# Kernel tuning notes

Measured on AMD Instinct MI355X. Metric: run time of the kernel, lower is better.

Reference implementation:

```python
import jax, jax.numpy as jnp
import numpy as np

D_MODEL, D_K, D_V, HEAD = 512, 512, 512, 8
SCALE = 1.0 / np.sqrt(D_K)  # torch code divides by sqrt(d_k) (full d_k, not head_dim)
NEG = -1.0e9


def setup_inputs() -> dict:
    key = jax.random.key(0)
    ks = jax.random.split(key, 10)
    B, S = 2, 4096
    x = jax.random.normal(ks[0], (B, S, D_MODEL), dtype=jnp.float32)
    mask = jax.random.randint(ks[1], (B, S), 0, 2, dtype=jnp.int32)
    s = 1.0 / np.sqrt(D_MODEL)
    Wq = jax.random.normal(ks[2], (D_MODEL, D_K), dtype=jnp.float32) * s
    bq = jnp.zeros((D_K,), jnp.float32)
    Wk = jax.random.normal(ks[3], (D_MODEL, D_K), dtype=jnp.float32) * s
    bk = jnp.zeros((D_K,), jnp.float32)
    Wv = jax.random.normal(ks[4], (D_MODEL, D_V), dtype=jnp.float32) * s
    bv = jnp.zeros((D_V,), jnp.float32)
    Wo = jax.random.normal(ks[5], (D_V, D_MODEL), dtype=jnp.float32) * s
    bo = jnp.zeros((D_MODEL,), jnp.float32)
    return {"x": x, "mask": mask, "Wq": Wq, "bq": bq, "Wk": Wk, "bk": bk,
            "Wv": Wv, "bv": bv, "Wo": Wo, "bo": bo}


def reference(x, mask, Wq, bq, Wk, bk, Wv, bv, Wo, bo):
    B, S, _ = x.shape
    hd_k = D_K // HEAD
    hd_v = D_V // HEAD
    # projections -> [B, H, S, hd]
    Q = (x @ Wq + bq).reshape(B, S, HEAD, hd_k).transpose(0, 2, 1, 3)
    K = (x @ Wk + bk).reshape(B, S, HEAD, hd_k).transpose(0, 2, 1, 3)
    V = (x @ Wv + bv).reshape(B, S, HEAD, hd_v).transpose(0, 2, 1, 3)
    # scores [B, H, S, S], scaled by 1/sqrt(d_k) (full d_k, faithful to source)
    scores = jnp.einsum('bhqd,bhkd->bhqk', Q, K) * SCALE
    m = (mask == 1)[:, None, None, :]  # [B,1,1,S]
    scores = jnp.where(m, NEG, scores)
    attn = jax.nn.softmax(scores, axis=-1)
    out = jnp.einsum('bhqk,bhkd->bhqd', attn, V)  # [B,H,S,hd_v]
    out = out.transpose(0, 2, 1, 3).reshape(B, S, D_V)
    return out @ Wo + bo
```

## Files before the change

### kernel.cpp

```cpp
#include <hip/hip_runtime.h>
#include <hip/hip_bf16.h>
#include <stdint.h>

typedef __attribute__((ext_vector_type(8))) short bf16x8;
typedef __attribute__((ext_vector_type(4))) float f32x4;
typedef __attribute__((ext_vector_type(16))) float f32x16;
typedef __attribute__((ext_vector_type(4))) unsigned int u32x4;

#define MFMA16(a, b, c) __builtin_amdgcn_mfma_f32_16x16x32_bf16(a, b, c, 0, 0, 0)
#define MFMA32(a, b, c) __builtin_amdgcn_mfma_f32_32x32x16_bf16(a, b, c, 0, 0, 0)

constexpr float QSCALE = 0.04419417382415922f * 1.4426950408889634f;

__device__ __forceinline__ void gload_lds16(const void* g, void* l) {
  __builtin_amdgcn_global_load_lds((const __attribute__((address_space(1))) uint32_t*)g,
                                   (__attribute__((address_space(3))) uint32_t*)l, 16, 0, 0);
}
__device__ __forceinline__ bf16x8 lds_read_swz(const short* base, int row, int ch) {
  return *(const bf16x8*)((const char*)base + row * 128 + (((ch ^ row) & 7) << 4));
}
__device__ __forceinline__ short f2b(float f) {
  __hip_bfloat16 h = __float2bfloat16(f);
  return *reinterpret_cast<short*>(&h);
}
__device__ __forceinline__ float exp2fast(float x) {
#if __has_builtin(__builtin_amdgcn_exp2f)
  return __builtin_amdgcn_exp2f(x);
#else
  return exp2f(x);
#endif
}

__global__ void k_cvt_x(const float* __restrict__ x, short* __restrict__ xb) {
  const int i = blockIdx.x * 256 + threadIdx.x;
  const float4 v = ((const float4*)x)[i];
  short4 o;
  o.x = f2b(v.x); o.y = f2b(v.y); o.z = f2b(v.z); o.w = f2b(v.w);
  ((short4*)xb)[i] = o;
}

__global__ void k_cvt_w(const float* __restrict__ wq, const float* __restrict__ wk,
                        const float* __restrict__ wv, const float* __restrict__ wo,
                        short* __restrict__ wt) {
  const int gid = blockIdx.x * 256 + threadIdx.x;
  const int mat = gid >> 18;
  const int idx = gid & 262143;
  const int n = idx >> 9, k = idx & 511;
  const float* w = (mat == 0) ? wq : (mat == 1) ? wk : (mat == 2) ? wv : wo;
  wt[gid] = f2b(w[k * 512 + n]);
}

__global__ void k_scan(const int* __restrict__ mask, int* __restrict__ perm,
                       int* __restrict__ cnt) {
  __shared__ int ws[16];
  const int b = blockIdx.x, tid = threadIdx.x;
  const int lane = tid & 63, w = tid >> 6;
  const int* m = mask + b * 4096;
  int v[4], s = 0;
#pragma unroll
  for (int j = 0; j < 4; ++j) { v[j] = (m[tid * 4 + j] == 0) ? 1 : 0; s += v[j]; }
  int sc = s;
  for (int d = 1; d < 64; d <<= 1) { int t = __shfl_up(sc, d); if (lane >= d) sc += t; }
  if (lane == 63) ws[w] = sc;
  __syncthreads();
  if (tid == 0) {
    int acc = 0;
    for (int i = 0; i < 16; ++i) { int t = ws[i]; ws[i] = acc; acc += t; }
    cnt[b] = acc;
  }
  __syncthreads();
  int pos = ws[w] + sc - s;
  int* p = perm + b * 4096;
#pragma unroll
  for (int j = 0; j < 4; ++j) { p[tid * 4 + j] = v[j] ? pos : -1; pos += v[j]; }
}

__global__ __launch_bounds__(256, 2) void k_gemmqkv(
    const short* __restrict__ A, const short* __restrict__ W,
    const float* __restrict__ bq, const float* __restrict__ bk,
    const float* __restrict__ bv, const int* __restrict__ perm,
    short* __restrict__ oq, short* __restrict__ ok, short* __restrict__ ov) {
  __shared__ short Asm[2][128 * 64];
  __shared__ short Bsm[2][128 * 64];
  const int tid = threadIdx.x;
  const int wave = tid >> 6, lane = tid & 63;
  const int lane15 = lane & 15, g = lane >> 4;
  const int wm = wave >> 1, wn = wave & 1;
  const int m0 = blockIdx.x * 128;
  const int n0 = blockIdx.y * 128;

  const char* Ag = (const char*)A + (size_t)m0 * 1024;
  const char* Bg = (const char*)W + (size_t)n0 * 1024;

  f32x4 acc[4][4] = {};

  auto stage = [&](int buf, int kt) {
    const int k0b = kt * 128;
#pragma unroll
    for (int q = 0; q < 4; ++q) {
      int s_ = (wave * 4 + q) * 64 + lane;
      int row = s_ >> 3, ch = s_ & 7;
      gload_lds16(Ag + (size_t)row * 1024 + k0b + (((ch ^ row) & 7) << 4),
                  (char*)&Asm[buf][0] + s_ * 16);
      gload_lds16(Bg + (size_t)row * 1024 + k0b + (((ch ^ row) & 7) << 4),
                  (char*)&Bsm[buf][0] + s_ * 16);
    }
  };

  stage(0, 0);
  asm volatile("s_waitcnt vmcnt(0)" ::: "memory");
  __syncthreads();

  for (int kt = 0; kt < 8; ++kt) {
    const int cur = kt & 1;
    if (kt < 7) stage(cur ^ 1, kt + 1);
#pragma unroll
    for (int kk = 0; kk < 2; ++kk) {
      bf16x8 af[4], bfr[4];
#pragma unroll
      for (int m = 0; m < 4; ++m)
        af[m] = lds_read_swz(&Asm[cur][0], wm * 64 + m * 16 + lane15, kk * 4 + g);
#pragma unroll
      for (int n = 0; n < 4; ++n)
        bfr[n] = lds_read_swz(&Bsm[cur][0], wn * 64 + n * 16 + lane15, kk * 4 + g);
      __builtin_amdgcn_s_setprio(1);
#pragma unroll
      for (int m = 0; m < 4; ++m)
#pragma unroll
        for (int n = 0; n < 4; ++n)
          acc[m][n] = MFMA16(af[m], bfr[n], acc[m][n]);
      __builtin_amdgcn_s_setprio(0);
    }
    asm volatile("s_waitcnt vmcnt(0)" ::: "memory");
    __syncthreads();
  }

#pragma unroll
  for (int nf = 0; nf < 4; ++nf) {
    const int col = n0 + wn * 64 + nf * 16 + lane15;
    const int mat = col >> 9, nn = col & 511;
    const int hh = nn >> 6, d = nn & 63;
    const float bias = ((mat == 0) ? bq : (mat == 1) ? bk : bv)[nn];
    const int dk = d >> 4, hb = (d >> 3) & 1, jj = d & 7;
#pragma unroll
    for (int mf = 0; mf < 4; ++mf) {
#pragma unroll
      for (int j = 0; j < 4; ++j) {
        const int rowg = m0 + wm * 64 + mf * 16 + g * 4 + j;
        const int b_ = rowg >> 12, sl = rowg & 4095;
        const size_t bh = (size_t)(b_ * 8 + hh);
        const float v = acc[mf][nf][j] + bias;
        if (mat == 0) {
          oq[bh * 262144 +
             (size_t)(((sl >> 5) * 4 + dk) * 64 + hb * 32 + (sl & 31)) * 8 + jj] =
              f2b(v * QSCALE);
        } else {
          const int pm_ = perm[b_ * 4096 + sl];
          if (pm_ >= 0) {
            const int t = pm_ >> 6, r = pm_ & 63;
            if (mat == 1) {
              ok[bh * 262144 +
                 (size_t)((t * 8 + dk * 2 + (r >> 5)) * 64 + hb * 32 + (r & 31)) * 8 + jj] =
                  f2b(v);
            } else {
              const int mm = (r & ~12) | (((r >> 2) & 1) << 3) | (((r >> 3) & 1) << 2);
              ov[bh * 262144 +
                 (size_t)((t * 8 + ((mm >> 4) & 3) * 2 + (d >> 5)) * 64 +
                          ((mm >> 3) & 1) * 32 + (d & 31)) * 8 + (mm & 7)] = f2b(v);
            }
          }
        }
      }
    }
  }
}

__global__ __launch_bounds__(256, 2) void k_gemmo(
    const short* __restrict__ A, const short* __restrict__ W,
    const float* __restrict__ bias, float* __restrict__ fo) {
  __shared__ short Asm[2][128 * 64];
  __shared__ short Bsm[2][64 * 64];
  const int tid = threadIdx.x;
  const int wave = tid >> 6, lane = tid & 63;
  const int lane15 = lane & 15, g = lane >> 4;
  const int wm = wave >> 1, wn = wave & 1;
  const int m0 = blockIdx.x * 128;
  const int n0 = blockIdx.y * 64;

  const char* Ag = (const char*)A + (size_t)m0 * 1024;
  const char* Bg = (const char*)W + (size_t)n0 * 1024;

  f32x4 acc[4][2] = {};

  auto stage = [&](int buf, int kt) {
    const int k0b = kt * 128;
#pragma unroll
    for (int q = 0; q < 4; ++q) {
      int s_ = (wave * 4 + q) * 64 + lane;
      int row = s_ >> 3, ch = s_ & 7;
      gload_lds16(Ag + (size_t)row * 1024 + k0b + (((ch ^ row) & 7) << 4),
                  (char*)&Asm[buf][0] + s_ * 16);
    }
#pragma unroll
    for (int q = 0; q < 2; ++q) {
      int s_ = (wave * 2 + q) * 64 + lane;
      int row = s_ >> 3, ch = s_ & 7;
      gload_lds16(Bg + (size_t)row * 1024 + k0b + (((ch ^ row) & 7) << 4),
                  (char*)&Bsm[buf][0] + s_ * 16);
    }
  };

  stage(0, 0);
  asm volatile("s_waitcnt vmcnt(0)" ::: "memory");
  __syncthreads();

  for (int kt = 0; kt < 8; ++kt) {
    const int cur = kt & 1;
    if (kt < 7) stage(cur ^ 1, kt + 1);
#pragma unroll
    for (int kk = 0; kk < 2; ++kk) {
      bf16x8 af[4], bfr[2];
#pragma unroll
      for (int m = 0; m < 4; ++m)
        af[m] = lds_read_swz(&Asm[cur][0], wm * 64 + m * 16 + lane15, kk * 4 + g);
#pragma unroll
      for (int n = 0; n < 2; ++n)
        bfr[n] = lds_read_swz(&Bsm[cur][0], wn * 32 + n * 16 + lane15, kk * 4 + g);
      __builtin_amdgcn_s_setprio(1);
#pragma unroll
      for (int m = 0; m < 4; ++m)
#pragma unroll
        for (int n = 0; n < 2; ++n)
          acc[m][n] = MFMA16(af[m], bfr[n], acc[m][n]);
      __builtin_amdgcn_s_setprio(0);
    }
    asm volatile("s_waitcnt vmcnt(0)" ::: "memory");
    __syncthreads();
  }

#pragma unroll
  for (int nf = 0; nf < 2; ++nf) {
    const int col = n0 + wn * 32 + nf * 16 + lane15;
    const float b = bias[col];
#pragma unroll
    for (int mf = 0; mf < 4; ++mf)
#pragma unroll
      for (int j = 0; j < 4; ++j) {
        const int rowg = m0 + wm * 64 + mf * 16 + g * 4 + j;
        fo[(size_t)rowg * 512 + col] = acc[mf][nf][j] + b;
      }
  }
}

__global__ __launch_bounds__(256, 2) void k_attn(
    const short* __restrict__ Qp, const short* __restrict__ Kp,
    const short* __restrict__ Vp, const int* __restrict__ cnt,
    short* __restrict__ out) {
  __shared__ short Ks[2][8][512];
  __shared__ short Vs[2][8][512];

  const int tid = threadIdx.x;
  const int wave = tid >> 6, lane = tid & 63;
  const int l31 = lane & 31, h = lane >> 5;
  const int bid = blockIdx.x;
  const int sid = (bid & 7) * 64 + (bid >> 3);
  const int qt = sid & 31, bh = sid >> 5;
  const int b = bh >> 3, hh = bh & 7;
  const int qb = qt * 4 + wave;

  const short* Qg = Qp + (size_t)bh * 262144;
  const short* Kg = Kp + (size_t)bh * 262144;
  const short* Vg = Vp + (size_t)bh * 262144;

  bf16x8 qreg[4];
#pragma unroll
  for (int dk = 0; dk < 4; ++dk)
    qreg[dk] = *(const bf16x8*)(Qg + ((size_t)(qb * 4 + dk) * 64 + lane) * 8);

  const int cn = cnt[b];
  const int nt = max(1, (cn + 63) >> 6);
  const int lim = cn - (nt - 1) * 64;

  auto stage = [&](int buf, int t) {
#pragma unroll
    for (int q = 0; q < 2; ++q) {
      const int u = wave * 2 + q;
      gload_lds16(Kg + ((size_t)(t * 8 + u) * 64 + lane) * 8, &Ks[buf][u][lane * 8]);
      gload_lds16(Vg + ((size_t)(t * 8 + u) * 64 + lane) * 8, &Vs[buf][u][lane * 8]);
    }
  };
  auto ldsK = [&](int buf, int u) { return *(const bf16x8*)&Ks[buf][u][lane * 8]; };
  auto ldsV = [&](int buf, int u) { return *(const bf16x8*)&Vs[buf][u][lane * 8]; };

  f32x16 o0 = {}, o1 = {};
  float l_ = 0.f;

  stage(0, 0);
  __syncthreads();

  for (int t = 0; t < nt; ++t) {
    const int cur = t & 1;
    if (t + 1 < nt) stage(cur ^ 1, t + 1);

    f32x16 s0v = {}, s1v = {};
    __builtin_amdgcn_s_setprio(1);
#pragma unroll
    for (int dk = 0; dk < 4; ++dk) {
      s0v = MFMA32(ldsK(cur, 2 * dk), qreg[dk], s0v);
      s1v = MFMA32(ldsK(cur, 2 * dk + 1), qreg[dk], s1v);
    }
    __builtin_amdgcn_s_setprio(0);

    if (t == nt - 1 && lim < 64) {
#pragma unroll
      for (int i = 0; i < 16; ++i) {
        const int r0 = (i & 3) + 8 * (i >> 2) + 4 * h;
        if (r0 >= lim) s0v[i] = -1e30f;
        if (r0 + 32 >= lim) s1v[i] = -1e30f;
      }
    }

    unsigned int wA[8], wB[8];
    float ts = 0.f;
#pragma unroll
    for (int j2 = 0; j2 < 8; ++j2) {
      float a0 = exp2fast(s0v[2 * j2]);
      float a1 = exp2fast(s0v[2 * j2 + 1]);
      float b0 = exp2fast(s1v[2 * j2]);
      float b1 = exp2fast(s1v[2 * j2 + 1]);
      ts += (a0 + a1) + (b0 + b1);
      asm("v_cvt_pk_bf16_f32 %0, %1, %2" : "=v"(wA[j2]) : "v"(a0), "v"(a1));
      asm("v_cvt_pk_bf16_f32 %0, %1, %2" : "=v"(wB[j2]) : "v"(b0), "v"(b1));
    }
    l_ += ts;

    __builtin_amdgcn_s_setprio(1);
#pragma unroll
    for (int s = 0; s < 4; ++s) {
      const bf16x8 v0 = ldsV(cur, 2 * s);
      const bf16x8 v1 = ldsV(cur, 2 * s + 1);
      const unsigned int* w = (s < 2) ? wA : wB;
      union PU { u32x4 u; bf16x8 f; } pu;
      pu.u[0] = w[4 * (s & 1) + 0];
      pu.u[1] = w[4 * (s & 1) + 1];
      pu.u[2] = w[4 * (s & 1) + 2];
      pu.u[3] = w[4 * (s & 1) + 3];
      o0 = MFMA32(v0, pu.f, o0);
      o1 = MFMA32(v1, pu.f, o1);
    }
    __builtin_amdgcn_s_setprio(0);

    __syncthreads();
  }

  l_ += __shfl_xor(l_, 32);
  const float inv = 1.0f / l_;
  short* og = out + (size_t)(b * 4096 + qb * 32 + l31) * 512 + hh * 64;
#pragma unroll
  for (int r2 = 0; r2 < 4; ++r2) {
    {
      const int base = 8 * r2 + 4 * h;
      short4 s4;
      s4.x = f2b(o0[4 * r2 + 0] * inv);
      s4.y = f2b(o0[4 * r2 + 1] * inv);
      s4.z = f2b(o0[4 * r2 + 2] * inv);
      s4.w = f2b(o0[4 * r2 + 3] * inv);
      *(short4*)(og + base) = s4;
    }
    {
      const int base = 32 + 8 * r2 + 4 * h;
      short4 s4;
      s4.x = f2b(o1[4 * r2 + 0] * inv);
      s4.y = f2b(o1[4 * r2 + 1] * inv);
      s4.z = f2b(o1[4 * r2 + 2] * inv);
      s4.w = f2b(o1[4 * r2 + 3] * inv);
      *(short4*)(og + base) = s4;
    }
  }
}

extern "C" void kernel_launch(void* const* d_in, const int* in_sizes, int n_in,
                              void* d_out, int out_size, void* d_ws, size_t ws_size,
                              hipStream_t stream) {
  const float* x  = (const float*)d_in[0];
  const int* mask = (const int*)d_in[1];
  const float* Wq = (const float*)d_in[2];
  const float* bq = (const float*)d_in[3];
  const float* Wk = (const float*)d_in[4];
  const float* bk = (const float*)d_in[5];
  const float* Wv = (const float*)d_in[6];
  const float* bv = (const float*)d_in[7];
  const float* Wo = (const float*)d_in[8];
  const float* bo = (const float*)d_in[9];
  float* out = (float*)d_out;

  short* xb   = (short*)d_ws;
  short* wt   = xb + (size_t)8192 * 512;
  short* qws  = wt + (size_t)4 * 512 * 512;
  short* kws  = qws + (size_t)8192 * 512;
  short* vws  = kws + (size_t)8192 * 512;
  short* aout = vws + (size_t)8192 * 512;
  int* perm   = (int*)(aout + (size_t)8192 * 512);
  int* cntw   = perm + 8192;

  k_cvt_x<<<4096, 256, 0, stream>>>(x, xb);
  k_cvt_w<<<4096, 256, 0, stream>>>(Wq, Wk, Wv, Wo, wt);
  k_scan<<<2, 1024, 0, stream>>>(mask, perm, cntw);
  k_gemmqkv<<<dim3(64, 12), 256, 0, stream>>>(xb, wt, bq, bk, bv, perm, qws, kws, vws);
  k_attn<<<512, 256, 0, stream>>>(qws, kws, vws, cntw, aout);
  k_gemmo<<<dim3(64, 8), 256, 0, stream>>>(aout, wt + (size_t)3 * 512 * 512, bo, out);
}
```

Measured before the change: 180.4 us.

## Transpose MFMA operands for vectorized epilogue stores and tile weight conversion

The GEMM kernels swap the MFMA A/B operands so each lane holds four consecutive output columns, which lets the epilogues emit float4/short4 stores and float4 bias loads instead of scattered scalar ones. The per-row perm lookup is hoisted out of the column loop. The weight conversion kernel is rewritten to transpose through a padded shared-memory tile so both its reads and writes are coalesced. The V scatter path stays partly scalar, and the new address math has to match the layouts the attention kernel expects.

```diff
diff --git a/kernel.cpp b/kernel.cpp
--- a/kernel.cpp
+++ b/kernel.cpp
@@ -42,12 +42,23 @@
 __global__ void k_cvt_w(const float* __restrict__ wq, const float* __restrict__ wk,
                         const float* __restrict__ wv, const float* __restrict__ wo,
                         short* __restrict__ wt) {
-  const int gid = blockIdx.x * 256 + threadIdx.x;
-  const int mat = gid >> 18;
-  const int idx = gid & 262143;
-  const int n = idx >> 9, k = idx & 511;
+  __shared__ float tile[64][65];
+  const int mat = blockIdx.x >> 6;
+  const int t6 = blockIdx.x & 63;
+  const int k0 = (t6 >> 3) * 64, n0 = (t6 & 7) * 64;
   const float* w = (mat == 0) ? wq : (mat == 1) ? wk : (mat == 2) ? wv : wo;
-  wt[gid] = f2b(w[k * 512 + n]);
+  const int c = threadIdx.x & 63, r4 = threadIdx.x >> 6;
+#pragma unroll
+  for (int p = 0; p < 16; ++p) {
+    const int r = p * 4 + r4;
+    tile[r][c] = w[(k0 + r) * 512 + n0 + c];
+  }
+  __syncthreads();
+#pragma unroll
+  for (int p = 0; p < 16; ++p) {
+    const int r = p * 4 + r4;
+    wt[mat * 262144 + (n0 + r) * 512 + k0 + c] = f2b(tile[c][r]);
+  }
 }
 
 __global__ void k_scan(const int* __restrict__ mask, int* __restrict__ perm,
@@ -128,47 +139,52 @@
       for (int m = 0; m < 4; ++m)
 #pragma unroll
         for (int n = 0; n < 4; ++n)
-          acc[m][n] = MFMA16(af[m], bfr[n], acc[m][n]);
+          acc[m][n] = MFMA16(bfr[n], af[m], acc[m][n]);
       __builtin_amdgcn_s_setprio(0);
     }
     asm volatile("s_waitcnt vmcnt(0)" ::: "memory");
     __syncthreads();
   }
 
-#pragma unroll
-  for (int nf = 0; nf < 4; ++nf) {
-    const int col = n0 + wn * 64 + nf * 16 + lane15;
-    const int mat = col >> 9, nn = col & 511;
-    const int hh = nn >> 6, d = nn & 63;
-    const float bias = ((mat == 0) ? bq : (mat == 1) ? bk : bv)[nn];
-    const int dk = d >> 4, hb = (d >> 3) & 1, jj = d & 7;
-#pragma unroll
-    for (int mf = 0; mf < 4; ++mf) {
-#pragma unroll
-      for (int j = 0; j < 4; ++j) {
-        const int rowg = m0 + wm * 64 + mf * 16 + g * 4 + j;
-        const int b_ = rowg >> 12, sl = rowg & 4095;
-        const size_t bh = (size_t)(b_ * 8 + hh);
-        const float v = acc[mf][nf][j] + bias;
-        if (mat == 0) {
-          oq[bh * 262144 +
-             (size_t)(((sl >> 5) * 4 + dk) * 64 + hb * 32 + (sl & 31)) * 8 + jj] =
-              f2b(v * QSCALE);
+  const int mat = blockIdx.y >> 2;
+  const float* bptr = (mat == 0) ? bq : (mat == 1) ? bk : bv;
+  const int hh = ((n0 & 511) >> 6) + wn;
+  const int hb = g >> 1, j4 = (g & 1) * 4;
+
+#pragma unroll
+  for (int mf = 0; mf < 4; ++mf) {
+    const int rowg = m0 + wm * 64 + mf * 16 + lane15;
+    const int b_ = rowg >> 12, sl = rowg & 4095;
+    const size_t bh = (size_t)(b_ * 8 + hh);
+    int pm_ = 0;
+    if (mat != 0) pm_ = perm[b_ * 4096 + sl];
+#pragma unroll
+    for (int nf = 0; nf < 4; ++nf) {
+      const int nn = (n0 & 511) + wn * 64 + nf * 16 + g * 4;
+      const float4 b4 = *(const float4*)(bptr + nn);
+      const float v0 = acc[mf][nf][0] + b4.x;
+      const float v1 = acc[mf][nf][1] + b4.y;
+      const float v2 = acc[mf][nf][2] + b4.z;
+      const float v3 = acc[mf][nf][3] + b4.w;
+      if (mat == 0) {
+        short4 s4;
+        s4.x = f2b(v0 * QSCALE); s4.y = f2b(v1 * QSCALE);
+        s4.z = f2b(v2 * QSCALE); s4.w = f2b(v3 * QSCALE);
+        *(short4*)(oq + bh * 262144 +
+                   (size_t)(((sl >> 5) * 4 + nf) * 64 + hb * 32 + (sl & 31)) * 8 + j4) = s4;
+      } else if (pm_ >= 0) {
+        const int t = pm_ >> 6, r = pm_ & 63;
+        if (mat == 1) {
+          short4 s4;
+          s4.x = f2b(v0); s4.y = f2b(v1); s4.z = f2b(v2); s4.w = f2b(v3);
+          *(short4*)(ok + bh * 262144 +
+                     (size_t)((t * 8 + nf * 2 + (r >> 5)) * 64 + hb * 32 + (r & 31)) * 8 + j4) = s4;
         } else {
-          const int pm_ = perm[b_ * 4096 + sl];
-          if (pm_ >= 0) {
-            const int t = pm_ >> 6, r = pm_ & 63;
-            if (mat == 1) {
-              ok[bh * 262144 +
-                 (size_t)((t * 8 + dk * 2 + (r >> 5)) * 64 + hb * 32 + (r & 31)) * 8 + jj] =
-                  f2b(v);
-            } else {
-              const int mm = (r & ~12) | (((r >> 2) & 1) << 3) | (((r >> 3) & 1) << 2);
-              ov[bh * 262144 +
-                 (size_t)((t * 8 + ((mm >> 4) & 3) * 2 + (d >> 5)) * 64 +
-                          ((mm >> 3) & 1) * 32 + (d & 31)) * 8 + (mm & 7)] = f2b(v);
-            }
-          }
+          const int mm = (r & ~12) | (((r >> 2) & 1) << 3) | (((r >> 3) & 1) << 2);
+          short* base = ov + bh * 262144 +
+                        (size_t)((t * 8 + ((mm >> 4) & 3) * 2 + (nf >> 1)) * 64 +
+                                 ((mm >> 3) & 1) * 32 + (nf & 1) * 16 + g * 4) * 8 + (mm & 7);
+          base[0] = f2b(v0); base[8] = f2b(v1); base[16] = f2b(v2); base[24] = f2b(v3);
         }
       }
     }
@@ -231,7 +247,7 @@
       for (int m = 0; m < 4; ++m)
 #pragma unroll
         for (int n = 0; n < 2; ++n)
-          acc[m][n] = MFMA16(af[m], bfr[n], acc[m][n]);
+          acc[m][n] = MFMA16(bfr[n], af[m], acc[m][n]);
       __builtin_amdgcn_s_setprio(0);
     }
     asm volatile("s_waitcnt vmcnt(0)" ::: "memory");
@@ -239,16 +255,19 @@
   }
 
 #pragma unroll
-  for (int nf = 0; nf < 2; ++nf) {
-    const int col = n0 + wn * 32 + nf * 16 + lane15;
-    const float b = bias[col];
-#pragma unroll
-    for (int mf = 0; mf < 4; ++mf)
-#pragma unroll
-      for (int j = 0; j < 4; ++j) {
-        const int rowg = m0 + wm * 64 + mf * 16 + g * 4 + j;
-        fo[(size_t)rowg * 512 + col] = acc[mf][nf][j] + b;
-      }
+  for (int mf = 0; mf < 4; ++mf) {
+    const int rowg = m0 + wm * 64 + mf * 16 + lane15;
+#pragma unroll
+    for (int nf = 0; nf < 2; ++nf) {
+      const int cb = n0 + wn * 32 + nf * 16 + g * 4;
+      const float4 b4 = *(const float4*)(bias + cb);
+      float4 o4;
+      o4.x = acc[mf][nf][0] + b4.x;
+      o4.y = acc[mf][nf][1] + b4.y;
+      o4.z = acc[mf][nf][2] + b4.z;
+      o4.w = acc[mf][nf][3] + b4.w;
+      *(float4*)(fo + (size_t)rowg * 512 + cb) = o4;
+    }
   }
 }
 
@@ -404,7 +423,7 @@
   int* cntw   = perm + 8192;
 
   k_cvt_x<<<4096, 256, 0, stream>>>(x, xb);
-  k_cvt_w<<<4096, 256, 0, stream>>>(Wq, Wk, Wv, Wo, wt);
+  k_cvt_w<<<256, 256, 0, stream>>>(Wq, Wk, Wv, Wo, wt);
   k_scan<<<2, 1024, 0, stream>>>(mask, perm, cntw);
   k_gemmqkv<<<dim3(64, 12), 256, 0, stream>>>(xb, wt, bq, bk, bv, perm, qws, kws, vws);
   k_attn<<<512, 256, 0, stream>>>(qws, kws, vws, cntw, aout);
```

After: 166.9 us. 1.08x faster.
